# Kernel tuning notes

Hardware: AMD Instinct MI355X
Metric: run time of the kernel (lower is better)

The kernel has to match this reference:

```python
import jax, jax.numpy as jnp
import numpy as np

B, T, D, H = 4, 2048, 1024, 16
HD = D // H  # 64
LOCAL_CTX, BLOCKSIZE, VERTSIZE = 256, 1, 16
STRIDE = LOCAL_CTX // BLOCKSIZE  # 256


def build_fixed_mask(n):
    # num_verts == 1 branch of generate_fixed_attention_mask
    layout = np.zeros((n, n), dtype=np.bool_)
    # vertical stripes: top `vertsize` indices of each stride block
    for idx in range(STRIDE - VERTSIZE, STRIDE):
        layout[:, idx::STRIDE] = True
    rows = np.arange(n)
    # local: each query attends to its own stride-block
    same_block = (rows[:, None] // STRIDE) == (rows[None, :] // STRIDE)
    layout |= same_block
    # causal: zero out k > q
    layout &= rows[None, :] <= rows[:, None]
    return layout


def setup_inputs() -> dict:
    key = jax.random.key(0)
    k1, k2, k3, k4, k5 = jax.random.split(key, 5)
    s = 0.02
    return {
        "x": jax.random.normal(k1, (B, T, D), dtype=jnp.float32),
        "Wqkv": jax.random.normal(k2, (D, 3 * D), dtype=jnp.float32) * s,
        "bqkv": jax.random.normal(k3, (3 * D,), dtype=jnp.float32) * s,
        "Wproj": jax.random.normal(k4, (D, D), dtype=jnp.float32) * s,
        "bproj": jax.random.normal(k5, (D,), dtype=jnp.float32) * s,
        "mask": jnp.asarray(build_fixed_mask(T)),
    }


def reference(x, Wqkv, bqkv, Wproj, bproj, mask):
    b, t, _ = x.shape
    qkv = (x @ Wqkv + bqkv).reshape(b, t, 3, H, HD)
    # (B,T,3,H,HD) -> (B,H,T,HD) per component
    q = qkv[:, :, 0].transpose(0, 2, 1, 3)
    k = qkv[:, :, 1].transpose(0, 2, 1, 3)
    v = qkv[:, :, 2].transpose(0, 2, 1, 3)
    att = jnp.einsum("bhqd,bhkd->bhqk", q, k) * (1.0 / jnp.sqrt(jnp.float32(HD)))
    att = jnp.where(mask[:t, :t], att, -jnp.inf)
    att = jax.nn.softmax(att, axis=-1)
    y = jnp.einsum("bhqk,bhkd->bhqd", att, v)
    y = y.transpose(0, 2, 1, 3).reshape(b, t, D)
    return y @ Wproj + bproj
```

## Files before the change

### kernel.cpp

```cpp
#include <hip/hip_runtime.h>
#include <cstdint>
#include <cstddef>

typedef unsigned short u16;
typedef __attribute__((ext_vector_type(8))) short short8;
typedef __attribute__((ext_vector_type(4))) float f32x4;
typedef __attribute__((ext_vector_type(4))) unsigned short u16x4;

#define B_ 4
#define T_ 2048
#define D_ 1024
#define H_ 16
#define HD_ 64

__device__ __forceinline__ u16 f2bf(float f) {
  union { float f; unsigned i; } v; v.f = f;
  unsigned r = (v.i + 0x7FFFu + ((v.i >> 16) & 1u)) >> 16;
  return (u16)r;
}

__device__ __forceinline__ void load_lds16(const void* g, void* l) {
  __builtin_amdgcn_global_load_lds(
      (const __attribute__((address_space(1))) void*)g,
      (__attribute__((address_space(3))) void*)l, 16, 0, 0);
}

#define RBAR() asm volatile("s_barrier" ::: "memory")
#define VMC(n) asm volatile("s_waitcnt vmcnt(" #n ")" ::: "memory")

__global__ __launch_bounds__(256)
void pre_all(const float* __restrict__ x, u16* __restrict__ xb,
             const float* __restrict__ Wqkv, u16* __restrict__ WqkvT,
             const float* __restrict__ Wproj, u16* __restrict__ WprojT) {
  __shared__ u16 t[32][33];
  const int bid = blockIdx.x;
  const int tid = threadIdx.x;
  if (bid < 8192) {
    const size_t i = ((size_t)bid * 256 + tid) * 4;
    const f32x4 v = *(const f32x4*)(x + i);
    u16x4 o;
#pragma unroll
    for (int r = 0; r < 4; ++r) o[r] = f2bf(v[r]);
    *(u16x4*)(xb + i) = o;
    return;
  }
  const float* src; u16* dst; int R, C, bx, by;
  if (bid < 11264) {
    const int tb = bid - 8192;
    bx = tb % 96; by = tb / 96; src = Wqkv; dst = WqkvT; R = 1024; C = 3072;
  } else {
    const int tb = bid - 11264;
    bx = tb & 31; by = tb >> 5; src = Wproj; dst = WprojT; R = 1024; C = 1024;
  }
  const int c0 = bx * 32, r0 = by * 32;
  const int lr = tid >> 5, lc = tid & 31;
#pragma unroll
  for (int p = 0; p < 4; ++p)
    t[lr + p * 8][lc] = f2bf(src[(size_t)(r0 + lr + p * 8) * C + c0 + lc]);
  __syncthreads();
#pragma unroll
  for (int p = 0; p < 4; ++p)
    dst[(size_t)(c0 + lr + p * 8) * R + r0 + lc] = t[lc][lr + p * 8];
}

template <int EPI>
__global__ __launch_bounds__(256)
void gemm_db(const u16* __restrict__ A, const u16* __restrict__ Bt,
             const float* __restrict__ bias, int K, int N,
             void* __restrict__ o0v, u16* __restrict__ o1, u16* __restrict__ o2) {
  __shared__ u16 As[2][4096];
  __shared__ u16 Bs[2][4096];
  const int tid = threadIdx.x;
  const int lane = tid & 63;
  const int w = tid >> 6;
  const int q = lane >> 4, col = lane & 15;

  const int nbx = gridDim.x;
  const int id = blockIdx.y * nbx + blockIdx.x;
  const int nwg = nbx * gridDim.y;
  const int sid = (id & 7) * (nwg >> 3) + (id >> 3);
  const int m0 = (sid / nbx) * 128, n0 = (sid % nbx) * 128;

  const int wm = (w >> 1) * 64, wn = (w & 1) * 64;

  const int srow = tid >> 2;
  const int cb8 = ((tid & 3) ^ ((tid >> 3) & 3)) << 3;
  const u16* Ap = A + (size_t)(m0 + srow) * K + cb8;
  const u16* Bp = Bt + (size_t)(n0 + srow) * K + cb8;

  const int rs = (q ^ ((col >> 1) & 3)) << 3;

  f32x4 acc[4][4] = {};

  auto STAGE = [&](int b, int kb) {
    load_lds16(Ap + kb, &As[b][tid * 8]);
    load_lds16(Ap + (size_t)64 * K + kb, &As[b][2048 + tid * 8]);
    load_lds16(Bp + kb, &Bs[b][tid * 8]);
    load_lds16(Bp + (size_t)64 * K + kb, &Bs[b][2048 + tid * 8]);
  };

  const int NT = K >> 5;
  STAGE(0, 0);

  for (int t = 0; t < NT; ++t) {
    const int b = t & 1;
    if (t + 1 < NT) {
      STAGE(b ^ 1, (t + 1) << 5);
      VMC(4);
    } else {
      VMC(0);
    }
    RBAR();
    short8 af[4], bfr[4];
#pragma unroll
    for (int i = 0; i < 4; ++i)
      af[i] = *(const short8*)&As[b][(wm + i * 16 + col) * 32 + rs];
#pragma unroll
    for (int j = 0; j < 4; ++j)
      bfr[j] = *(const short8*)&Bs[b][(wn + j * 16 + col) * 32 + rs];
#pragma unroll
    for (int i = 0; i < 4; ++i)
#pragma unroll
      for (int j = 0; j < 4; ++j)
        acc[i][j] = __builtin_amdgcn_mfma_f32_16x16x32_bf16(af[i], bfr[j], acc[i][j], 0, 0, 0);
    RBAR();
  }

#pragma unroll
  for (int j = 0; j < 4; ++j) {
    const int n = n0 + wn + j * 16 + col;
    const float bv = bias[n];
    if constexpr (EPI == 0) {
      u16* q0p = (u16*)o0v;
      const int c = n >> 10, rem = n & 1023, hh = rem >> 6, dd = rem & 63;
#pragma unroll
      for (int i = 0; i < 4; ++i) {
        const int mrow = m0 + wm + i * 16 + q * 4;
        const int b = mrow >> 11, t = mrow & 2047;
        const int bh = b * H_ + hh;
        if (c == 0) {
#pragma unroll
          for (int r = 0; r < 4; ++r)
            q0p[((size_t)bh * T_ + t + r) * HD_ + dd] = f2bf((acc[i][j][r] + bv) * 0.125f);
        } else if (c == 1) {
#pragma unroll
          for (int r = 0; r < 4; ++r)
            o1[((size_t)bh * T_ + t + r) * HD_ + dd] = f2bf(acc[i][j][r] + bv);
        } else {
          u16x4 pk;
#pragma unroll
          for (int r = 0; r < 4; ++r) pk[r] = f2bf(acc[i][j][r] + bv);
          *(u16x4*)&o2[((size_t)bh * HD_ + dd) * T_ + t] = pk;
        }
      }
    } else {
      float* outp = (float*)o0v;
#pragma unroll
      for (int i = 0; i < 4; ++i) {
        const int mrow = m0 + wm + i * 16 + q * 4;
#pragma unroll
        for (int r = 0; r < 4; ++r)
          outp[(size_t)(mrow + r) * N + n] = acc[i][j][r] + bv;
      }
    }
  }
}

__global__ __launch_bounds__(256)
void sparse_attn(const u16* __restrict__ Qb, const u16* __restrict__ Kb,
                 const u16* __restrict__ Vt, u16* __restrict__ Y) {
  __shared__ char smem[20480];
  u16* Pall = (u16*)smem;
  float* Obuf = (float*)smem;

  const int tid = threadIdx.x, lane = tid & 63, w = tid >> 6;
  const int q = lane >> 4, col = lane & 15;
  const int bh = blockIdx.x, qt = blockIdx.y;
  const int b = bh >> 4, hh = bh & 15;
  const int qb = qt >> 2;
  const int rb = (qt & 3) * 64;
  const int qg = qt * 64;
  const u16* Qh = Qb + (size_t)bh * T_ * HD_;
  const u16* Kh = Kb + (size_t)bh * T_ * HD_;
  const u16* Vh = Vt + (size_t)bh * HD_ * T_;

  short8 qf[4][2];
#pragma unroll
  for (int i = 0; i < 4; ++i)
#pragma unroll
    for (int h2 = 0; h2 < 2; ++h2)
      qf[i][h2] = *(const short8*)&Qh[(size_t)(qg + i * 16 + col) * HD_ + h2 * 32 + q * 8];

  f32x4 o[4][4] = {};
  f32x4 lI[4] = {};
  const short8 ones = {0x3F80, 0x3F80, 0x3F80, 0x3F80, 0x3F80, 0x3F80, 0x3F80, 0x3F80};

  u16* P = Pall + w * 2560;

  const int ns = (qb + 1) >> 1;
  const int L = ns + 2 * (qt & 3) + 2;

  auto params = [&](int j, int& k0, int& k1, bool& mask1, int& localc) {
    if (j < ns) {
      k0 = (2 * j) * 256 + 240; k1 = k0 + 256;
      mask1 = (2 * j + 1 == qb); localc = -1;
    } else {
      const int c = j - ns;
      k0 = qb * 256 + c * 32; k1 = k0 + 16;
      mask1 = false; localc = c * 32;
    }
  };
  auto ldK = [&](int k0, int k1, short8* kf) {
    kf[0] = *(const short8*)&Kh[(size_t)(k0 + col) * HD_ + q * 8];
    kf[1] = *(const short8*)&Kh[(size_t)(k0 + col) * HD_ + 32 + q * 8];
    kf[2] = *(const short8*)&Kh[(size_t)(k1 + col) * HD_ + q * 8];
    kf[3] = *(const short8*)&Kh[(size_t)(k1 + col) * HD_ + 32 + q * 8];
  };

  int k0 = 0, k1 = 0, localc = -1;
  bool mask1 = false;
  short8 kf[4];
  if (w < L) { params(w, k0, k1, mask1, localc); ldK(k0, k1, kf); }

  for (int j = w; j < L; j += 4) {
    const int kvb = (q < 2) ? (k0 + q * 8) : (k1 + (q - 2) * 8);
    short8 vf[4];
#pragma unroll
    for (int dt = 0; dt < 4; ++dt)
      vf[dt] = *(const short8*)&Vh[(size_t)(dt * 16 + col) * T_ + kvb];
    int nk0 = 0, nk1 = 0, nlocalc = -1;
    bool nmask1 = false;
    short8 nkf[4];
    const bool hn = (j + 4) < L;
    if (hn) { params(j + 4, nk0, nk1, nmask1, nlocalc); ldK(nk0, nk1, nkf); }

#pragma unroll
    for (int rt = 0; rt < 4; ++rt) {
      f32x4 z = {0.f, 0.f, 0.f, 0.f};
      f32x4 s0 = __builtin_amdgcn_mfma_f32_16x16x32_bf16(qf[rt][0], kf[0], z, 0, 0, 0);
      s0 = __builtin_amdgcn_mfma_f32_16x16x32_bf16(qf[rt][1], kf[1], s0, 0, 0, 0);
      f32x4 s1 = __builtin_amdgcn_mfma_f32_16x16x32_bf16(qf[rt][0], kf[2], z, 0, 0, 0);
      s1 = __builtin_amdgcn_mfma_f32_16x16x32_bf16(qf[rt][1], kf[3], s1, 0, 0, 0);
#pragma unroll
      for (int r = 0; r < 4; ++r) {
        float p0 = __expf(s0[r]);
        float p1 = mask1 ? 0.f : __expf(s1[r]);
        if (localc >= 0) {
          const int qr = rb + rt * 16 + q * 4 + r;
          if (localc + col > qr) p0 = 0.f;
          if (localc + 16 + col > qr) p1 = 0.f;
        }
        P[(rt * 16 + q * 4 + r) * 40 + col] = f2bf(p0);
        P[(rt * 16 + q * 4 + r) * 40 + 16 + col] = f2bf(p1);
      }
    }
    asm volatile("s_waitcnt lgkmcnt(0)" ::: "memory");
    short8 pf[4];
#pragma unroll
    for (int rt = 0; rt < 4; ++rt)
      pf[rt] = *(const short8*)&P[(rt * 16 + col) * 40 + q * 8];
#pragma unroll
    for (int rt = 0; rt < 4; ++rt) {
#pragma unroll
      for (int dt = 0; dt < 4; ++dt)
        o[rt][dt] = __builtin_amdgcn_mfma_f32_16x16x32_bf16(pf[rt], vf[dt], o[rt][dt], 0, 0, 0);
      lI[rt] = __builtin_amdgcn_mfma_f32_16x16x32_bf16(pf[rt], ones, lI[rt], 0, 0, 0);
    }
    if (hn) {
      k0 = nk0; k1 = nk1; mask1 = nmask1; localc = nlocalc;
      kf[0] = nkf[0]; kf[1] = nkf[1]; kf[2] = nkf[2]; kf[3] = nkf[3];
    }
  }

#pragma unroll
  for (int rt = 0; rt < 4; ++rt) {
    __syncthreads();
#pragma unroll
    for (int dt = 0; dt < 4; ++dt)
      *(f32x4*)&Obuf[(w * 65 + dt * 16 + col) * 16 + q * 4] = o[rt][dt];
    if (col == 0)
      *(f32x4*)&Obuf[(w * 65 + 64) * 16 + q * 4] = lI[rt];
    __syncthreads();
    f32x4 acc = {0.f, 0.f, 0.f, 0.f};
    f32x4 lt = {0.f, 0.f, 0.f, 0.f};
#pragma unroll
    for (int w2 = 0; w2 < 4; ++w2) {
      acc += *(const f32x4*)&Obuf[(w2 * 65 + w * 16 + col) * 16 + q * 4];
      lt += *(const f32x4*)&Obuf[(w2 * 65 + 64) * 16 + q * 4];
    }
#pragma unroll
    for (int r = 0; r < 4; ++r) {
      const int trow = qg + rt * 16 + q * 4 + r;
      Y[((size_t)(b * T_ + trow)) * D_ + hh * HD_ + w * 16 + col] = f2bf(acc[r] / lt[r]);
    }
  }
}

extern "C" void kernel_launch(void* const* d_in, const int* in_sizes, int n_in,
                              void* d_out, int out_size, void* d_ws, size_t ws_size,
                              hipStream_t stream) {
  const float* x = (const float*)d_in[0];
  const float* Wqkv = (const float*)d_in[1];
  const float* bqkv = (const float*)d_in[2];
  const float* Wproj = (const float*)d_in[3];
  const float* bproj = (const float*)d_in[4];
  float* out = (float*)d_out;

  char* ws = (char*)d_ws;
  u16* xb     = (u16*)(ws + 0);
  u16* WqkvT  = (u16*)(ws + 16777216);
  u16* WprojT = (u16*)(ws + 23068672);
  u16* Qb     = (u16*)(ws + 25165824);
  u16* Kb     = (u16*)(ws + 41943040);
  u16* Vt     = (u16*)(ws + 58720256);
  u16* Y      = (u16*)(ws + 75497472);

  pre_all<<<dim3(12288), 256, 0, stream>>>(x, xb, Wqkv, WqkvT, Wproj, WprojT);
  gemm_db<0><<<dim3(24, 64), 256, 0, stream>>>(xb, WqkvT, bqkv, 1024, 3072, Qb, Kb, Vt);
  sparse_attn<<<dim3(64, 32), 256, 0, stream>>>(Qb, Kb, Vt, Y);
  gemm_db<1><<<dim3(8, 64), 256, 0, stream>>>(Y, WprojT, bproj, 1024, 1024, out, nullptr, nullptr);
}
```

Measured before the change: 241.2 us.

## Split attention rows across warps and keep P in registers via bpermute

Each wavefront now owns 16 query rows and walks every key chunk for them, where before all four wavefronts shared 64 rows and split the key chunks. This removes the cross-wave LDS reduction and its barriers at the end. The score matmul is transposed (K as A operand), so P can be packed with v_cvt_pk_bf16 and shuffled into MFMA operand layout with ds_bpermute instead of a round trip through LDS. The cost is that each wave loads all K/V chunks itself, so there is less K/V reuse across waves and the per-wave loop is longer and serial, with work per wave now uneven across rows.

```diff
diff --git a/kernel.cpp b/kernel.cpp
--- a/kernel.cpp
+++ b/kernel.cpp
@@ -17,6 +17,12 @@
   union { float f; unsigned i; } v; v.f = f;
   unsigned r = (v.i + 0x7FFFu + ((v.i >> 16) & 1u)) >> 16;
   return (u16)r;
+}
+
+__device__ __forceinline__ unsigned cvt_pk_bf16(float lo, float hi) {
+  unsigned r;
+  asm("v_cvt_pk_bf16_f32 %0, %1, %2" : "=v"(r) : "v"(lo), "v"(hi));
+  return r;
 }
 
 __device__ __forceinline__ void load_lds16(const void* g, void* l) {
@@ -169,36 +175,29 @@
 __global__ __launch_bounds__(256)
 void sparse_attn(const u16* __restrict__ Qb, const u16* __restrict__ Kb,
                  const u16* __restrict__ Vt, u16* __restrict__ Y) {
-  __shared__ char smem[20480];
-  u16* Pall = (u16*)smem;
-  float* Obuf = (float*)smem;
-
   const int tid = threadIdx.x, lane = tid & 63, w = tid >> 6;
   const int q = lane >> 4, col = lane & 15;
   const int bh = blockIdx.x, qt = blockIdx.y;
   const int b = bh >> 4, hh = bh & 15;
   const int qb = qt >> 2;
-  const int rb = (qt & 3) * 64;
-  const int qg = qt * 64;
+  const int rbw = (qt & 3) * 64 + w * 16;
+  const int rowg = qt * 64 + w * 16;
   const u16* Qh = Qb + (size_t)bh * T_ * HD_;
   const u16* Kh = Kb + (size_t)bh * T_ * HD_;
   const u16* Vh = Vt + (size_t)bh * HD_ * T_;
 
-  short8 qf[4][2];
-#pragma unroll
-  for (int i = 0; i < 4; ++i)
-#pragma unroll
-    for (int h2 = 0; h2 < 2; ++h2)
-      qf[i][h2] = *(const short8*)&Qh[(size_t)(qg + i * 16 + col) * HD_ + h2 * 32 + q * 8];
-
-  f32x4 o[4][4] = {};
-  f32x4 lI[4] = {};
+  short8 qf[2];
+#pragma unroll
+  for (int h = 0; h < 2; ++h)
+    qf[h] = *(const short8*)&Qh[(size_t)(rowg + col) * HD_ + h * 32 + q * 8];
+
+  f32x4 o[4] = {};
+  f32x4 lac = {};
+
   const short8 ones = {0x3F80, 0x3F80, 0x3F80, 0x3F80, 0x3F80, 0x3F80, 0x3F80, 0x3F80};
 
-  u16* P = Pall + w * 2560;
-
   const int ns = (qb + 1) >> 1;
-  const int L = ns + 2 * (qt & 3) + 2;
+  const int L = ns + (rbw >> 5) + 1;
 
   auto params = [&](int j, int& k0, int& k1, bool& mask1, int& localc) {
     if (j < ns) {
@@ -217,82 +216,82 @@
     kf[3] = *(const short8*)&Kh[(size_t)(k1 + col) * HD_ + 32 + q * 8];
   };
 
-  int k0 = 0, k1 = 0, localc = -1;
-  bool mask1 = false;
+  int k0, k1, localc;
+  bool mask1;
   short8 kf[4];
-  if (w < L) { params(w, k0, k1, mask1, localc); ldK(k0, k1, kf); }
-
-  for (int j = w; j < L; j += 4) {
+  params(0, k0, k1, mask1, localc);
+  ldK(k0, k1, kf);
+
+  const int bpa = (((lane & 15) | ((lane & 16) << 1)) << 2);
+  const f32x4 z = {0.f, 0.f, 0.f, 0.f};
+
+  for (int j = 0; j < L; ++j) {
     const int kvb = (q < 2) ? (k0 + q * 8) : (k1 + (q - 2) * 8);
     short8 vf[4];
 #pragma unroll
     for (int dt = 0; dt < 4; ++dt)
       vf[dt] = *(const short8*)&Vh[(size_t)(dt * 16 + col) * T_ + kvb];
-    int nk0 = 0, nk1 = 0, nlocalc = -1;
-    bool nmask1 = false;
-    short8 nkf[4];
-    const bool hn = (j + 4) < L;
-    if (hn) { params(j + 4, nk0, nk1, nmask1, nlocalc); ldK(nk0, nk1, nkf); }
-
-#pragma unroll
-    for (int rt = 0; rt < 4; ++rt) {
-      f32x4 z = {0.f, 0.f, 0.f, 0.f};
-      f32x4 s0 = __builtin_amdgcn_mfma_f32_16x16x32_bf16(qf[rt][0], kf[0], z, 0, 0, 0);
-      s0 = __builtin_amdgcn_mfma_f32_16x16x32_bf16(qf[rt][1], kf[1], s0, 0, 0, 0);
-      f32x4 s1 = __builtin_amdgcn_mfma_f32_16x16x32_bf16(qf[rt][0], kf[2], z, 0, 0, 0);
-      s1 = __builtin_amdgcn_mfma_f32_16x16x32_bf16(qf[rt][1], kf[3], s1, 0, 0, 0);
-#pragma unroll
-      for (int r = 0; r < 4; ++r) {
-        float p0 = __expf(s0[r]);
-        float p1 = mask1 ? 0.f : __expf(s1[r]);
-        if (localc >= 0) {
-          const int qr = rb + rt * 16 + q * 4 + r;
-          if (localc + col > qr) p0 = 0.f;
-          if (localc + 16 + col > qr) p1 = 0.f;
-        }
-        P[(rt * 16 + q * 4 + r) * 40 + col] = f2bf(p0);
-        P[(rt * 16 + q * 4 + r) * 40 + 16 + col] = f2bf(p1);
+
+    const bool cmask1 = mask1;
+    const int clocalc = localc;
+
+    f32x4 s0 = __builtin_amdgcn_mfma_f32_16x16x32_bf16(kf[0], qf[0], z, 0, 0, 0);
+    s0 = __builtin_amdgcn_mfma_f32_16x16x32_bf16(kf[1], qf[1], s0, 0, 0, 0);
+    f32x4 s1 = __builtin_amdgcn_mfma_f32_16x16x32_bf16(kf[2], qf[0], z, 0, 0, 0);
+    s1 = __builtin_amdgcn_mfma_f32_16x16x32_bf16(kf[3], qf[1], s1, 0, 0, 0);
+
+    const bool hn = (j + 1) < L;
+    if (hn) {
+      params(j + 1, k0, k1, mask1, localc);
+      ldK(k0, k1, kf);
+    }
+
+    float p0[4], p1[4];
+#pragma unroll
+    for (int r = 0; r < 4; ++r) {
+      p0[r] = __expf(s0[r]);
+      p1[r] = cmask1 ? 0.f : __expf(s1[r]);
+      if (clocalc >= 0) {
+        const int qr = rbw + col;
+        if (clocalc + q * 4 + r > qr) p0[r] = 0.f;
+        if (clocalc + 16 + q * 4 + r > qr) p1[r] = 0.f;
       }
     }
-    asm volatile("s_waitcnt lgkmcnt(0)" ::: "memory");
-    short8 pf[4];
-#pragma unroll
-    for (int rt = 0; rt < 4; ++rt)
-      pf[rt] = *(const short8*)&P[(rt * 16 + col) * 40 + q * 8];
-#pragma unroll
-    for (int rt = 0; rt < 4; ++rt) {
-#pragma unroll
-      for (int dt = 0; dt < 4; ++dt)
-        o[rt][dt] = __builtin_amdgcn_mfma_f32_16x16x32_bf16(pf[rt], vf[dt], o[rt][dt], 0, 0, 0);
-      lI[rt] = __builtin_amdgcn_mfma_f32_16x16x32_bf16(pf[rt], ones, lI[rt], 0, 0, 0);
-    }
-    if (hn) {
-      k0 = nk0; k1 = nk1; mask1 = nmask1; localc = nlocalc;
-      kf[0] = nkf[0]; kf[1] = nkf[1]; kf[2] = nkf[2]; kf[3] = nkf[3];
-    }
-  }
-
-#pragma unroll
-  for (int rt = 0; rt < 4; ++rt) {
-    __syncthreads();
+
+    const unsigned c0 = cvt_pk_bf16(p0[0], p0[1]);
+    const unsigned c1 = cvt_pk_bf16(p0[2], p0[3]);
+    const unsigned c2 = cvt_pk_bf16(p1[0], p1[1]);
+    const unsigned c3 = cvt_pk_bf16(p1[2], p1[3]);
+    const int t0a = __builtin_amdgcn_ds_bpermute(bpa, (int)c0);
+    const int t0b = __builtin_amdgcn_ds_bpermute(bpa, (int)c2);
+    const int t1a = __builtin_amdgcn_ds_bpermute(bpa, (int)c1);
+    const int t1b = __builtin_amdgcn_ds_bpermute(bpa, (int)c3);
+    const int t2a = __builtin_amdgcn_ds_bpermute(bpa + 64, (int)c0);
+    const int t2b = __builtin_amdgcn_ds_bpermute(bpa + 64, (int)c2);
+    const int t3a = __builtin_amdgcn_ds_bpermute(bpa + 64, (int)c1);
+    const int t3b = __builtin_amdgcn_ds_bpermute(bpa + 64, (int)c3);
+    union { unsigned u[4]; short8 v; } pb;
+    const bool lo32 = lane < 32;
+    pb.u[0] = lo32 ? (unsigned)t0a : (unsigned)t0b;
+    pb.u[1] = lo32 ? (unsigned)t1a : (unsigned)t1b;
+    pb.u[2] = lo32 ? (unsigned)t2a : (unsigned)t2b;
+    pb.u[3] = lo32 ? (unsigned)t3a : (unsigned)t3b;
+
 #pragma unroll
     for (int dt = 0; dt < 4; ++dt)
-      *(f32x4*)&Obuf[(w * 65 + dt * 16 + col) * 16 + q * 4] = o[rt][dt];
-    if (col == 0)
-      *(f32x4*)&Obuf[(w * 65 + 64) * 16 + q * 4] = lI[rt];
-    __syncthreads();
-    f32x4 acc = {0.f, 0.f, 0.f, 0.f};
-    f32x4 lt = {0.f, 0.f, 0.f, 0.f};
-#pragma unroll
-    for (int w2 = 0; w2 < 4; ++w2) {
-      acc += *(const f32x4*)&Obuf[(w2 * 65 + w * 16 + col) * 16 + q * 4];
-      lt += *(const f32x4*)&Obuf[(w2 * 65 + 64) * 16 + q * 4];
-    }
-#pragma unroll
-    for (int r = 0; r < 4; ++r) {
-      const int trow = qg + rt * 16 + q * 4 + r;
-      Y[((size_t)(b * T_ + trow)) * D_ + hh * HD_ + w * 16 + col] = f2bf(acc[r] / lt[r]);
-    }
+      o[dt] = __builtin_amdgcn_mfma_f32_16x16x32_bf16(vf[dt], pb.v, o[dt], 0, 0, 0);
+    lac = __builtin_amdgcn_mfma_f32_16x16x32_bf16(ones, pb.v, lac, 0, 0, 0);
+  }
+
+  const float inv = 1.0f / lac[0];
+  const int trow = rowg + col;
+  u16* Yr = Y + ((size_t)(b * T_ + trow)) * D_ + hh * HD_ + q * 4;
+#pragma unroll
+  for (int dt = 0; dt < 4; ++dt) {
+    u16x4 pk;
+#pragma unroll
+    for (int r = 0; r < 4; ++r) pk[r] = f2bf(o[dt][r] * inv);
+    *(u16x4*)&Yr[dt * 16] = pk;
   }
 }
 
```

Result: slower. 262.2 us (+8.7%).
